# Performance work log

Measured on AMD Instinct MI355X. Metric: run time of the kernel, lower is better.

Reference implementation:

```python
import jax, jax.numpy as jnp
import numpy as np
import math

D_MODEL = 1024
RPN_D = 256
SUP_HW = 20  # support feature map is 20x20 -> 400 tokens


def _positional_encoding(max_len, d_model):
    pos = np.arange(max_len, dtype=np.float32)[:, None]
    div = np.exp(np.arange(0, d_model, 2, dtype=np.float32) * -(math.log(10000.0) / float(d_model)))
    pe = np.zeros((max_len, d_model), dtype=np.float32)
    pe[:, 0::2] = np.sin(pos * div)
    pe[:, 1::2] = np.cos(pos * div)
    return jnp.asarray(pe)


def setup_inputs() -> dict:
    key = jax.random.key(0)
    ks = jax.random.split(key, 6)
    B, S, H = 4, 5, 4
    fh, fw = 64, 64
    base_feat = jax.random.normal(ks[0], (B, D_MODEL, fh, fw), dtype=jnp.float32)
    support_feat = jax.random.normal(ks[1], (B, S, D_MODEL, SUP_HW, SUP_HW), dtype=jnp.float32)
    Qw = jax.random.normal(ks[2], (H, RPN_D, D_MODEL), dtype=jnp.float32) * 0.01
    Qb = jnp.zeros((H, RPN_D), dtype=jnp.float32)
    Kw = jax.random.normal(ks[3], (H, RPN_D, D_MODEL), dtype=jnp.float32) * 0.01
    Kb = jnp.zeros((H, RPN_D), dtype=jnp.float32)
    Mw = jax.random.normal(ks[4], (D_MODEL, H * D_MODEL), dtype=jnp.float32) * 0.02
    Mb = jnp.zeros((D_MODEL,), dtype=jnp.float32)
    return {"base_feat": base_feat, "support_feat": support_feat,
            "Qw": Qw, "Qb": Qb, "Kw": Kw, "Kb": Kb, "Mw": Mw, "Mb": Mb}


def reference(base_feat, support_feat, Qw, Qb, Kw, Kb, Mw, Mb):
    B, C, fh, fw = base_feat.shape
    S = support_feat.shape[1]
    H = Qw.shape[0]
    Lq = fh * fw
    Lk = SUP_HW * SUP_HW

    # support_mat: [S, B, Lk, C]  (transpose(0,1) then flatten spatial, then transpose)
    support_mat = jnp.transpose(support_feat, (1, 0, 2, 3, 4)).reshape(S, B, C, Lk)
    support_mat = jnp.transpose(support_mat, (0, 1, 3, 2))
    # query_mat: [B, Lq, C]
    query_mat = jnp.transpose(base_feat.reshape(B, C, Lq), (0, 2, 1))

    pe = _positional_encoding(400, D_MODEL)[:Lk]  # [Lk, C]
    s_mat = support_mat + pe[None, None]          # [S, B, Lk, C]

    # per-head projections (q is independent of shot, compute once)
    q = jnp.einsum('blc,hdc->hbld', query_mat, Qw) + Qb[:, None, None, :]   # [H,B,Lq,d]
    k = jnp.einsum('sbkc,hdc->hsbkd', s_mat, Kw) + Kb[:, None, None, None, :]  # [H,S,B,Lk,d]

    scores = jnp.einsum('hbld,hsbkd->hsblk', q, k) / math.sqrt(RPN_D)  # [H,S,B,Lq,Lk]
    attn = jax.nn.softmax(scores, axis=-1)
    z = jnp.einsum('hsblk,sbkc->hsblc', attn, s_mat)  # [H,S,B,Lq,C]

    # shot_mode == 'mean'
    z = jnp.mean(z, axis=1)  # [H,B,Lq,C]

    # concat heads along feature dim (head order preserved): [B,Lq,H*C]
    att = jnp.transpose(z, (1, 2, 0, 3)).reshape(B, Lq, H * C)
    att = jax.nn.relu(att @ Mw.T + Mb)  # [B,Lq,C]

    att = jnp.transpose(att, (0, 2, 1)).reshape(B, C, fh, fw)
    # attention_type == 'product'
    correlation_feat = base_feat * att
    return correlation_feat
```

## Files before the change

### kernel.cpp

```cpp
#include <hip/hip_runtime.h>
#include <stdint.h>

#define DEVI __device__ __forceinline__

typedef __attribute__((ext_vector_type(8))) short bf16x8;
typedef __attribute__((ext_vector_type(4))) float f32x4;
typedef __attribute__((ext_vector_type(4))) unsigned short us4;
typedef unsigned short u16;

constexpr int B_ = 4, S_ = 5, H_ = 4, C_ = 1024, D_ = 256;
constexpr int LQ = 4096, LK = 400, LKP = 448, LKM = 512;

DEVI u16 f2b(float f){
  uint32_t x = __float_as_uint(f);
  uint32_t r = (x + 0x7FFFu + ((x >> 16) & 1u)) >> 16;
  return (u16)r;
}

typedef __attribute__((address_space(1))) const void ASG;
typedef __attribute__((address_space(3))) void ASL;
DEVI void gload16(const void* g, void* l){
  __builtin_amdgcn_global_load_lds((ASG*)g, (ASL*)l, 16, 0, 0);
}

__global__ __launch_bounds__(256) void k_cvt(const float* __restrict__ s, u16* __restrict__ d, int n4){
  int i = blockIdx.x*256 + threadIdx.x;
  if (i >= n4) return;
  float4 v = ((const float4*)s)[i];
  us4 o; o.x = f2b(v.x); o.y = f2b(v.y); o.z = f2b(v.z); o.w = f2b(v.w);
  *(us4*)(d + (size_t)i*4) = o;
}

__global__ __launch_bounds__(256) void k_transpose_x(const float* __restrict__ base, u16* __restrict__ Xb){
  __shared__ float t[32][33];
  int l0 = blockIdx.x*32, c0 = blockIdx.y*32, b = blockIdx.z;
  int tx = threadIdx.x & 31, ty = threadIdx.x >> 5;
  const float* src = base + ((size_t)b*C_ + c0)*LQ + l0;
  #pragma unroll
  for (int i=0;i<4;i++){ int cc = ty + i*8; t[cc][tx] = src[(size_t)cc*LQ + tx]; }
  __syncthreads();
  u16* dst = Xb + ((size_t)b*LQ + l0)*C_ + c0;
  #pragma unroll
  for (int i=0;i<4;i++){ int ll = ty + i*8; dst[(size_t)ll*C_ + tx] = f2b(t[tx][ll]); }
}

__global__ __launch_bounds__(256) void k_build_smat(const float* __restrict__ sup, u16* __restrict__ kc){
  __shared__ float t[32][33];
  int p0 = blockIdx.x*32, c0 = blockIdx.y*32;
  int s = blockIdx.z / B_, b = blockIdx.z % B_;
  int tx = threadIdx.x & 31, ty = threadIdx.x >> 5;
  const float* src = sup + ((size_t)(b*S_ + s)*C_ + c0)*LK + p0;
  #pragma unroll
  for (int i=0;i<4;i++){
    int cc = ty + i*8;
    int p = p0 + tx;
    int c = c0 + cc;
    float v = 0.f;
    if (p < LK){
      v = src[(size_t)cc*LK + tx];
      float dv = expf(-(float)(c & ~1) * (9.210340371976184f / 1024.f));
      float arg = (float)p * dv;
      v += (c & 1) ? cosf(arg) : sinf(arg);
    }
    t[cc][tx] = v;
  }
  __syncthreads();
  u16* dkc = kc + ((size_t)((s*B_ + b)*LKM + p0))*C_ + c0;
  #pragma unroll
  for (int i=0;i<4;i++){ int pp = ty + i*8; dkc[(size_t)pp*C_ + tx] = f2b(t[tx][pp]); }
}

DEVI void stage_half(const u16* P, int64_t ld, u16* dst, int wid, int r8, int s8){
  #pragma unroll
  for (int it=0; it<2; ++it){
    int ck = wid + it*8;
    gload16(P + (size_t)(ck*8 + r8)*ld + s8*8, dst + ck*512);
  }
}
DEVI bf16x8 ldsread(const u16* base, int row, int kk, int lane){
  int sl = ((kk<<2) + (lane>>4)) ^ (row & 7);
  return *(const bf16x8*)&base[row*64 + sl*8];
}

template<int CEPI, bool FIRST, bool FINAL, bool BIAS>
__global__ __launch_bounds__(512,1) void k8(
    const u16* __restrict__ A, const u16* __restrict__ Bm, void* __restrict__ Cm,
    const float* __restrict__ bias, const float* __restrict__ basep, const float* __restrict__ Mb,
    int tilesM, int64_t lda, int64_t ldb, int64_t ldc,
    int spc, int NT, int64_t aChunk, int64_t bChunk,
    int bdiv, int64_t aS0, int64_t aS1, int64_t bS0, int64_t bS1,
    int64_t cS0, int64_t cS1, int biasS0, float scale, int Nmax, int swz){
  __shared__ __align__(16) u16 lds[2][2][16384];
  int tid = threadIdx.x, lane = tid & 63, wid = tid >> 6;
  int bx = blockIdx.x;
  if (swz) bx = (bx & 7) * (gridDim.x >> 3) + (bx >> 3);
  int mt = bx % tilesM, ntile = bx / tilesM;
  int z = blockIdx.y, i0 = z / bdiv, i1 = z % bdiv;
  const u16* Ab = A + i0*aS0 + i1*aS1 + (size_t)mt*256*lda;
  const u16* Bb = Bm + i0*bS0 + i1*bS1 + (size_t)ntile*256*ldb;
  int r8 = lane >> 3, s8 = (lane & 7) ^ r8;
  int wr = wid >> 2, wc = wid & 3;

  f32x4 acc[8][4];
  #pragma unroll
  for (int i=0;i<8;i++)
    #pragma unroll
    for (int j=0;j<4;j++) acc[i][j] = (f32x4){0.f,0.f,0.f,0.f};

  const u16 *ApS = Ab, *BpS = Bb; int cs = 0;
  stage_half(ApS,                   lda, &lds[0][0][0],    wid, r8, s8);
  stage_half(ApS + (size_t)128*lda, lda, &lds[0][0][8192], wid, r8, s8);
  stage_half(BpS,                   ldb, &lds[0][1][0],    wid, r8, s8);
  stage_half(BpS + (size_t)128*ldb, ldb, &lds[0][1][8192], wid, r8, s8);
  ApS += 64; BpS += 64;
  if (++cs == spc){ cs = 0; ApS += aChunk - (int64_t)spc*64; BpS += bChunk - (int64_t)spc*64; }

  for (int t = 0; t < NT; ++t){
    int cur = t & 1, nxt = cur ^ 1;
    bool pf = (t + 1 < NT);
    const u16* lA = &lds[cur][0][0];
    const u16* lB = &lds[cur][1][0];
    if (pf){
      u16* sA = &lds[nxt][0][0];
      u16* sB = &lds[nxt][1][0];
      stage_half(ApS,                   lda, sA,        wid, r8, s8);
      stage_half(ApS + (size_t)128*lda, lda, sA + 8192, wid, r8, s8);
      stage_half(BpS,                   ldb, sB,        wid, r8, s8);
      stage_half(BpS + (size_t)128*ldb, ldb, sB + 8192, wid, r8, s8);
      ApS += 64; BpS += 64;
      if (++cs == spc){ cs = 0; ApS += aChunk - (int64_t)spc*64; BpS += bChunk - (int64_t)spc*64; }
      asm volatile("s_waitcnt vmcnt(8)" ::: "memory");
    } else {
      asm volatile("s_waitcnt vmcnt(0)" ::: "memory");
    }
    asm volatile("s_barrier" ::: "memory");

    bf16x8 bfr[4][2];
    #pragma unroll
    for (int jn=0;jn<4;jn++)
      #pragma unroll
      for (int kk=0;kk<2;kk++)
        bfr[jn][kk] = ldsread(lB, wc*64 + jn*16 + (lane & 15), kk, lane);

    #pragma unroll
    for (int p = 0; p < 4; ++p){
      bf16x8 af[2][2];
      #pragma unroll
      for (int dm=0;dm<2;dm++)
        #pragma unroll
        for (int kk=0;kk<2;kk++)
          af[dm][kk] = ldsread(lA, wr*128 + (p*2+dm)*16 + (lane & 15), kk, lane);
      __builtin_amdgcn_s_setprio(1);
      #pragma unroll
      for (int dm=0;dm<2;dm++)
        #pragma unroll
        for (int jn=0;jn<4;jn++)
          #pragma unroll
          for (int kk=0;kk<2;kk++)
            acc[p*2+dm][jn] = __builtin_amdgcn_mfma_f32_16x16x32_bf16(af[dm][kk], bfr[jn][kk], acc[p*2+dm][jn], 0,0,0);
      __builtin_amdgcn_s_setprio(0);
    }
    asm volatile("s_barrier" ::: "memory");
  }

  int g = lane >> 4, c16 = lane & 15;
  if constexpr (CEPI == 0){
    u16* Cb = (u16*)Cm + i0*cS0 + i1*cS1;
    #pragma unroll
    for (int jn=0;jn<4;jn++){
      int n = ntile*256 + wc*64 + jn*16 + c16;
      if (n >= Nmax) continue;
      float bv = 0.f;
      if (BIAS) bv = bias[(size_t)i0*biasS0 + n];
      #pragma unroll
      for (int im=0;im<8;im++){
        int m = mt*256 + wr*128 + im*16 + g*4;
        #pragma unroll
        for (int r=0;r<4;r++)
          Cb[(size_t)(m + r)*ldc + n] = f2b((acc[im][jn][r] + bv)*scale);
      }
    }
  } else {
    float* Cb = (float*)Cm + i0*cS0 + i1*cS1;
    const float* Bs = basep + i0*cS0 + i1*cS1;
    #pragma unroll
    for (int jn=0;jn<4;jn++){
      int n = ntile*256 + wc*64 + jn*16 + c16;
      float mbv = 0.f;
      if (FINAL) mbv = Mb[n];
      #pragma unroll
      for (int im=0;im<8;im++){
        int m = mt*256 + wr*128 + im*16 + g*4;
        float* p = Cb + (size_t)n*ldc + m;
        float4 v;
        v.x = acc[im][jn][0]; v.y = acc[im][jn][1]; v.z = acc[im][jn][2]; v.w = acc[im][jn][3];
        if (!FIRST){
          float4 old = *(const float4*)p;
          v.x += old.x; v.y += old.y; v.z += old.z; v.w += old.w;
        }
        if (FINAL){
          float4 bs = *(const float4*)(Bs + (size_t)n*ldc + m);
          v.x = bs.x * fmaxf(0.2f*v.x + mbv, 0.f);
          v.y = bs.y * fmaxf(0.2f*v.y + mbv, 0.f);
          v.z = bs.z * fmaxf(0.2f*v.z + mbv, 0.f);
          v.w = bs.w * fmaxf(0.2f*v.w + mbv, 0.f);
        }
        *(float4*)p = v;
      }
    }
  }
}

__global__ __launch_bounds__(512) void k_scores(
    const u16* __restrict__ qws, const u16* __restrict__ kws,
    u16* __restrict__ attn, int h){
  __shared__ __align__(16) u16 lQ[128*64];
  __shared__ __align__(16) u16 lK[400*64];
  int tid = threadIdx.x, lane = tid & 63, wid = tid >> 6;
  int m0 = blockIdx.x * 128;
  int b = blockIdx.y;
  int s = blockIdx.z;
  const u16* Qp = qws + ((size_t)(h*B_ + b)*LQ + m0)*D_;
  const u16* Kp = kws + ((size_t)((h*S_ + s)*B_ + b))*((size_t)LKM*D_);
  int r8 = lane >> 3, s8 = (lane & 7) ^ r8;
  f32x4 acc[25];
  #pragma unroll
  for (int t=0;t<25;t++) acc[t] = (f32x4){0.f,0.f,0.f,0.f};
  int wm = wid * 16;
  for (int k0 = 0; k0 < 256; k0 += 64){
    __syncthreads();
    #pragma unroll
    for (int c = 0; c < 2; ++c){
      int cc = wid + c*8;
      int row = cc*8 + r8;
      gload16(Qp + (size_t)row*D_ + k0 + s8*8, &lQ[cc*512]);
    }
    for (int cc = wid; cc < 50; cc += 8){
      int row = cc*8 + r8;
      gload16(Kp + (size_t)row*D_ + k0 + s8*8, &lK[cc*512]);
    }
    __syncthreads();
    #pragma unroll
    for (int kk = 0; kk < 2; ++kk){
      int rowA = wm + (lane & 15);
      int slA = ((kk<<2) + (lane>>4)) ^ (rowA & 7);
      bf16x8 af = *(const bf16x8*)&lQ[rowA*64 + slA*8];
      #pragma unroll
      for (int t=0;t<25;t++){
        int rowB = t*16 + (lane & 15);
        int slB = ((kk<<2) + (lane>>4)) ^ (rowB & 7);
        bf16x8 bf = *(const bf16x8*)&lK[rowB*64 + slB*8];
        acc[t] = __builtin_amdgcn_mfma_f32_16x16x32_bf16(af, bf, acc[t], 0,0,0);
      }
    }
  }
  float mx[4] = {-1e30f,-1e30f,-1e30f,-1e30f};
  #pragma unroll
  for (int t=0;t<25;t++)
    #pragma unroll
    for (int r=0;r<4;r++) mx[r] = fmaxf(mx[r], acc[t][r]);
  #pragma unroll
  for (int r=0;r<4;r++){
    mx[r] = fmaxf(mx[r], __shfl_xor(mx[r], 1));
    mx[r] = fmaxf(mx[r], __shfl_xor(mx[r], 2));
    mx[r] = fmaxf(mx[r], __shfl_xor(mx[r], 4));
    mx[r] = fmaxf(mx[r], __shfl_xor(mx[r], 8));
  }
  float sm[4] = {0.f,0.f,0.f,0.f};
  #pragma unroll
  for (int t=0;t<25;t++)
    #pragma unroll
    for (int r=0;r<4;r++){ float e = __expf(acc[t][r] - mx[r]); acc[t][r] = e; sm[r] += e; }
  #pragma unroll
  for (int r=0;r<4;r++){
    sm[r] += __shfl_xor(sm[r], 1);
    sm[r] += __shfl_xor(sm[r], 2);
    sm[r] += __shfl_xor(sm[r], 4);
    sm[r] += __shfl_xor(sm[r], 8);
    sm[r] = 1.f / sm[r];
  }
  u16* ap = attn + ((size_t)((s*B_ + b)*LQ) + m0 + wm)*LKP;
  int g = lane >> 4, c16 = lane & 15;
  #pragma unroll
  for (int t=0;t<25;t++)
    #pragma unroll
    for (int r=0;r<4;r++)
      ap[(size_t)(g*4 + r)*LKP + t*16 + c16] = f2b(acc[t][r] * sm[r]);
  for (int t = lane; t < 16*48; t += 64){
    int rr = t / 48, cp = 400 + (t % 48);
    ap[(size_t)rr*LKP + cp] = 0;
  }
}

extern "C" void kernel_launch(void* const* d_in, const int* in_sizes, int n_in,
                              void* d_out, int out_size, void* d_ws, size_t ws_size,
                              hipStream_t stream){
  const float* base = (const float*)d_in[0];
  const float* sup  = (const float*)d_in[1];
  const float* Qw   = (const float*)d_in[2];
  const float* Qb   = (const float*)d_in[3];
  const float* Kw   = (const float*)d_in[4];
  const float* Kb   = (const float*)d_in[5];
  const float* Mw   = (const float*)d_in[6];
  const float* Mb   = (const float*)d_in[7];
  float* out = (float*)d_out;
  char* ws = (char*)d_ws;

  u16* wQw = (u16*)(ws + 0);
  u16* wKw = (u16*)(ws + 2097152);
  u16* wMw = (u16*)(ws + 4194304);
  u16* wKC = (u16*)(ws + 12582912);
  u16* wK  = (u16*)(ws + 33554432);
  u16* wQ  = (u16*)(ws + 54525952);
  u16* wVt = (u16*)(ws + 88080384);
  u16* wXb = (u16*)(ws + 106430464);
  u16* wATs = (u16*)(ws + 106430464);

  const int BIG = 1 << 30;

  k_cvt<<<1024, 256, 0, stream>>>(Qw, wQw, 262144);
  k_cvt<<<1024, 256, 0, stream>>>(Kw, wKw, 262144);
  k_cvt<<<4096, 256, 0, stream>>>(Mw, wMw, 1048576);
  k_transpose_x<<<dim3(128, 32, 4), 256, 0, stream>>>(base, wXb);
  k_build_smat<<<dim3(16, 32, 20), 256, 0, stream>>>(sup, wKC);

  k8<0,false,false,true><<<dim3(2, 80), 512, 0, stream>>>(
      wKC, wKw, wK, Kb, nullptr, nullptr,
      2, C_, C_, D_, 16, 16, 0, 0,
      20, 0, (int64_t)LKM*C_, (int64_t)D_*C_, 0,
      (int64_t)S_*B_*LKM*D_, (int64_t)LKM*D_, D_, 1.f, BIG, 0);

  k8<0,false,false,true><<<dim3(16, 16), 512, 0, stream>>>(
      wXb, wQw, wQ, Qb, nullptr, nullptr,
      16, C_, C_, D_, 16, 16, 0, 0,
      4, 0, (int64_t)LQ*C_, (int64_t)D_*C_, 0,
      (int64_t)B_*LQ*D_, (int64_t)LQ*D_, D_, 1.f/16.f, BIG, 1);

  for (int h = 0; h < H_; ++h){
    k8<0,false,false,false><<<dim3(8, 20), 512, 0, stream>>>(
        wMw + (size_t)h*C_, wKC, wVt, nullptr, nullptr, nullptr,
        4, (int64_t)H_*C_, C_, LKP, 16, 16, 0, 0,
        4, 0, 0, (int64_t)B_*LKM*C_, (int64_t)LKM*C_,
        (int64_t)B_*C_*LKP, (int64_t)C_*LKP, 0, 1.f, LKP, 0);

    k_scores<<<dim3(32, 4, 5), 512, 0, stream>>>(wQ, wK, wATs, h);

    if (h == 0){
      k8<1,true,false,false><<<dim3(64, 4), 512, 0, stream>>>(
          wATs, wVt, out, nullptr, base, Mb,
          16, LKP, LKP, LQ, 7, 35, (int64_t)B_*LQ*LKP, (int64_t)B_*C_*LKP,
          1, (int64_t)LQ*LKP, 0, (int64_t)C_*LKP, 0,
          (int64_t)C_*LQ, 0, 0, 1.f, BIG, 1);
    } else if (h < 3){
      k8<1,false,false,false><<<dim3(64, 4), 512, 0, stream>>>(
          wATs, wVt, out, nullptr, base, Mb,
          16, LKP, LKP, LQ, 7, 35, (int64_t)B_*LQ*LKP, (int64_t)B_*C_*LKP,
          1, (int64_t)LQ*LKP, 0, (int64_t)C_*LKP, 0,
          (int64_t)C_*LQ, 0, 0, 1.f, BIG, 1);
    } else {
      k8<1,false,true,false><<<dim3(64, 4), 512, 0, stream>>>(
          wATs, wVt, out, nullptr, base, Mb,
          16, LKP, LKP, LQ, 7, 35, (int64_t)B_*LQ*LKP, (int64_t)B_*C_*LKP,
          1, (int64_t)LQ*LKP, 0, (int64_t)C_*LKP, 0,
          (int64_t)C_*LQ, 0, 0, 1.f, BIG, 1);
    }
  }
}
```

Baseline: 799.9 us.

## Batch two heads per attention pass and shrink support padding to 448

The padded key length drops from 512 to 448 rows, which shrinks the K-projection and support buffers and lets the workspace be repacked. When the workspace is large enough, two heads are grouped per iteration. The V-projection and scores kernels then cover both heads in one launch, and the attention-times-V GEMM accumulates over both heads with twice the K chunks. This roughly halves the number of launches and the read-modify-write passes over the fp32 output. A new tile mapping (swz==2) groups M tiles by XCD for the big GEMM, and an Mmax guard skips the padded rows. The cost is a larger workspace requirement, with a fallback to one head per pass.

```diff
diff --git a/kernel.cpp b/kernel.cpp
--- a/kernel.cpp
+++ b/kernel.cpp
@@ -9,7 +9,7 @@
 typedef unsigned short u16;
 
 constexpr int B_ = 4, S_ = 5, H_ = 4, C_ = 1024, D_ = 256;
-constexpr int LQ = 4096, LK = 400, LKP = 448, LKM = 512;
+constexpr int LQ = 4096, LK = 400, LKP = 448;
 
 DEVI u16 f2b(float f){
   uint32_t x = __float_as_uint(f);
@@ -65,7 +65,7 @@
     t[cc][tx] = v;
   }
   __syncthreads();
-  u16* dkc = kc + ((size_t)((s*B_ + b)*LKM + p0))*C_ + c0;
+  u16* dkc = kc + ((size_t)((s*B_ + b)*LKP + p0))*C_ + c0;
   #pragma unroll
   for (int i=0;i<4;i++){ int pp = ty + i*8; dkc[(size_t)pp*C_ + tx] = f2b(t[tx][pp]); }
 }
@@ -89,12 +89,16 @@
     int tilesM, int64_t lda, int64_t ldb, int64_t ldc,
     int spc, int NT, int64_t aChunk, int64_t bChunk,
     int bdiv, int64_t aS0, int64_t aS1, int64_t bS0, int64_t bS1,
-    int64_t cS0, int64_t cS1, int biasS0, float scale, int Nmax, int swz){
+    int64_t cS0, int64_t cS1, int biasS0, float scale, int Nmax, int Mmax, int swz){
   __shared__ __align__(16) u16 lds[2][2][16384];
   int tid = threadIdx.x, lane = tid & 63, wid = tid >> 6;
   int bx = blockIdx.x;
-  if (swz) bx = (bx & 7) * (gridDim.x >> 3) + (bx >> 3);
-  int mt = bx % tilesM, ntile = bx / tilesM;
+  int mt, ntile;
+  if (swz == 2){ int x = bx & 7, j = bx >> 3; mt = 2*x + (j >> 2); ntile = j & 3; }
+  else {
+    if (swz == 1) bx = (bx & 7) * (gridDim.x >> 3) + (bx >> 3);
+    mt = bx % tilesM; ntile = bx / tilesM;
+  }
   int z = blockIdx.y, i0 = z / bdiv, i1 = z % bdiv;
   const u16* Ab = A + i0*aS0 + i1*aS1 + (size_t)mt*256*lda;
   const u16* Bb = Bm + i0*bS0 + i1*bS1 + (size_t)ntile*256*ldb;
@@ -175,6 +179,7 @@
       #pragma unroll
       for (int im=0;im<8;im++){
         int m = mt*256 + wr*128 + im*16 + g*4;
+        if (m >= Mmax) continue;
         #pragma unroll
         for (int r=0;r<4;r++)
           Cb[(size_t)(m + r)*ldc + n] = f2b((acc[im][jn][r] + bv)*scale);
@@ -213,15 +218,16 @@
 
 __global__ __launch_bounds__(512) void k_scores(
     const u16* __restrict__ qws, const u16* __restrict__ kws,
-    u16* __restrict__ attn, int h){
+    u16* __restrict__ attn, int h0){
   __shared__ __align__(16) u16 lQ[128*64];
   __shared__ __align__(16) u16 lK[400*64];
   int tid = threadIdx.x, lane = tid & 63, wid = tid >> 6;
   int m0 = blockIdx.x * 128;
   int b = blockIdx.y;
-  int s = blockIdx.z;
+  int zz = blockIdx.z;
+  int s = zz % 5, h = h0 + zz / 5;
   const u16* Qp = qws + ((size_t)(h*B_ + b)*LQ + m0)*D_;
-  const u16* Kp = kws + ((size_t)((h*S_ + s)*B_ + b))*((size_t)LKM*D_);
+  const u16* Kp = kws + ((size_t)((h*S_ + s)*B_ + b))*((size_t)LKP*D_);
   int r8 = lane >> 3, s8 = (lane & 7) ^ r8;
   f32x4 acc[25];
   #pragma unroll
@@ -279,7 +285,7 @@
     sm[r] += __shfl_xor(sm[r], 8);
     sm[r] = 1.f / sm[r];
   }
-  u16* ap = attn + ((size_t)((s*B_ + b)*LQ) + m0 + wm)*LKP;
+  u16* ap = attn + ((size_t)((zz*B_ + b)*LQ) + m0 + wm)*LKP;
   int g = lane >> 4, c16 = lane & 15;
   #pragma unroll
   for (int t=0;t<25;t++)
@@ -310,11 +316,14 @@
   u16* wKw = (u16*)(ws + 2097152);
   u16* wMw = (u16*)(ws + 4194304);
   u16* wKC = (u16*)(ws + 12582912);
-  u16* wK  = (u16*)(ws + 33554432);
-  u16* wQ  = (u16*)(ws + 54525952);
-  u16* wVt = (u16*)(ws + 88080384);
-  u16* wXb = (u16*)(ws + 106430464);
-  u16* wATs = (u16*)(ws + 106430464);
+  u16* wK  = (u16*)(ws + 30932992);
+  u16* wQ  = (u16*)(ws + 49283072);
+  u16* wVt = (u16*)(ws + 82837504);
+
+  const int GH = (ws_size >= 266338304ull) ? 2 : 1;
+  const int NG = H_ / GH;
+  u16* wAT = (u16*)(ws + 82837504 + (size_t)GH*18350080ull);
+  u16* wXb = wAT;
 
   const int BIG = 1 << 30;
 
@@ -322,47 +331,47 @@
   k_cvt<<<1024, 256, 0, stream>>>(Kw, wKw, 262144);
   k_cvt<<<4096, 256, 0, stream>>>(Mw, wMw, 1048576);
   k_transpose_x<<<dim3(128, 32, 4), 256, 0, stream>>>(base, wXb);
-  k_build_smat<<<dim3(16, 32, 20), 256, 0, stream>>>(sup, wKC);
+  k_build_smat<<<dim3(14, 32, 20), 256, 0, stream>>>(sup, wKC);
 
   k8<0,false,false,true><<<dim3(2, 80), 512, 0, stream>>>(
       wKC, wKw, wK, Kb, nullptr, nullptr,
-      2, C_, C_, D_, 16, 16, 0, 0,
-      20, 0, (int64_t)LKM*C_, (int64_t)D_*C_, 0,
-      (int64_t)S_*B_*LKM*D_, (int64_t)LKM*D_, D_, 1.f, BIG, 0);
+      2, C_, C_, D_, 16, 16, 1024, 1024,
+      20, 0, (int64_t)LKP*C_, (int64_t)D_*C_, 0,
+      (int64_t)S_*B_*LKP*D_, (int64_t)LKP*D_, D_, 1.f, BIG, LKP, 0);
 
   k8<0,false,false,true><<<dim3(16, 16), 512, 0, stream>>>(
       wXb, wQw, wQ, Qb, nullptr, nullptr,
-      16, C_, C_, D_, 16, 16, 0, 0,
+      16, C_, C_, D_, 16, 16, 1024, 1024,
       4, 0, (int64_t)LQ*C_, (int64_t)D_*C_, 0,
-      (int64_t)B_*LQ*D_, (int64_t)LQ*D_, D_, 1.f/16.f, BIG, 1);
-
-  for (int h = 0; h < H_; ++h){
-    k8<0,false,false,false><<<dim3(8, 20), 512, 0, stream>>>(
-        wMw + (size_t)h*C_, wKC, wVt, nullptr, nullptr, nullptr,
-        4, (int64_t)H_*C_, C_, LKP, 16, 16, 0, 0,
-        4, 0, 0, (int64_t)B_*LKM*C_, (int64_t)LKM*C_,
-        (int64_t)B_*C_*LKP, (int64_t)C_*LKP, 0, 1.f, LKP, 0);
-
-    k_scores<<<dim3(32, 4, 5), 512, 0, stream>>>(wQ, wK, wATs, h);
-
-    if (h == 0){
+      (int64_t)B_*LQ*D_, (int64_t)LQ*D_, D_, 1.f/16.f, BIG, BIG, 1);
+
+  for (int g = 0; g < NG; ++g){
+    k8<0,false,false,false><<<dim3(8, GH*20), 512, 0, stream>>>(
+        wMw + (size_t)(g*GH)*C_, wKC, wVt, nullptr, nullptr, nullptr,
+        4, (int64_t)H_*C_, C_, LKP, 16, 16, 1024, 1024,
+        20, (int64_t)C_, 0, 0, (int64_t)LKP*C_,
+        (int64_t)20*C_*LKP, (int64_t)C_*LKP, 0, 1.f, LKP, BIG, 0);
+
+    k_scores<<<dim3(32, 4, GH*5), 512, 0, stream>>>(wQ, wK, wAT, g*GH);
+
+    if (g == 0){
       k8<1,true,false,false><<<dim3(64, 4), 512, 0, stream>>>(
-          wATs, wVt, out, nullptr, base, Mb,
-          16, LKP, LKP, LQ, 7, 35, (int64_t)B_*LQ*LKP, (int64_t)B_*C_*LKP,
+          wAT, wVt, out, nullptr, base, Mb,
+          16, LKP, LKP, LQ, 7, GH*35, (int64_t)B_*LQ*LKP, (int64_t)B_*C_*LKP,
           1, (int64_t)LQ*LKP, 0, (int64_t)C_*LKP, 0,
-          (int64_t)C_*LQ, 0, 0, 1.f, BIG, 1);
-    } else if (h < 3){
+          (int64_t)C_*LQ, 0, 0, 1.f, BIG, BIG, 2);
+    } else if (g == NG - 1){
+      k8<1,false,true,false><<<dim3(64, 4), 512, 0, stream>>>(
+          wAT, wVt, out, nullptr, base, Mb,
+          16, LKP, LKP, LQ, 7, GH*35, (int64_t)B_*LQ*LKP, (int64_t)B_*C_*LKP,
+          1, (int64_t)LQ*LKP, 0, (int64_t)C_*LKP, 0,
+          (int64_t)C_*LQ, 0, 0, 1.f, BIG, BIG, 2);
+    } else {
       k8<1,false,false,false><<<dim3(64, 4), 512, 0, stream>>>(
-          wATs, wVt, out, nullptr, base, Mb,
-          16, LKP, LKP, LQ, 7, 35, (int64_t)B_*LQ*LKP, (int64_t)B_*C_*LKP,
+          wAT, wVt, out, nullptr, base, Mb,
+          16, LKP, LKP, LQ, 7, GH*35, (int64_t)B_*LQ*LKP, (int64_t)B_*C_*LKP,
           1, (int64_t)LQ*LKP, 0, (int64_t)C_*LKP, 0,
-          (int64_t)C_*LQ, 0, 0, 1.f, BIG, 1);
-    } else {
-      k8<1,false,true,false><<<dim3(64, 4), 512, 0, stream>>>(
-          wATs, wVt, out, nullptr, base, Mb,
-          16, LKP, LKP, LQ, 7, 35, (int64_t)B_*LQ*LKP, (int64_t)B_*C_*LKP,
-          1, (int64_t)LQ*LKP, 0, (int64_t)C_*LKP, 0,
-          (int64_t)C_*LQ, 0, 0, 1.f, BIG, 1);
-    }
-  }
-}
+          (int64_t)C_*LQ, 0, 0, 1.f, BIG, BIG, 2);
+    }
+  }
+}
```

Result: faster. 758.9 us (-5.1%).
